# Kernel tuning notes

Measured on AMD Instinct MI355X. Metric: run time of the kernel, lower is better.

The kernel has to match this reference:

```python
import jax, jax.numpy as jnp
import numpy as np
from functools import partial

@jax.custom_vjp
def binarize(w):
    # BinaryConnectDeterministic forward: sign(w)
    return jnp.sign(w)

def _bin_fwd(w):
    return jnp.sign(w), w

def _bin_bwd(w, g):
    # straight-through estimator: pass grad where |w| <= 1
    return (g * (jnp.abs(w) <= 1.0).astype(g.dtype),)

binarize.defvjp(_bin_fwd, _bin_bwd)

STRIDE = (1, 1)
PADDING = ((1, 1), (1, 1))
DILATION = (1, 1)
GROUPS = 1

def setup_inputs() -> dict:
    key = jax.random.key(0)
    k1, k2, k3 = jax.random.split(key, 3)
    x = jax.random.normal(k1, (32, 256, 56, 56), dtype=jnp.float32)
    # uniform(-1, 1) init as in reset_parameters
    weight = jax.random.uniform(k2, (256, 256, 3, 3), dtype=jnp.float32, minval=-1.0, maxval=1.0)
    bias = jax.random.uniform(k3, (256,), dtype=jnp.float32, minval=-1.0, maxval=1.0)
    return {"x": x, "weight": weight, "bias": bias}

def reference(x, weight, bias):
    w_bin = binarize(weight)  # {-1, 0, +1} weights (sign)
    out = jax.lax.conv_general_dilated(
        x, w_bin,
        window_strides=STRIDE,
        padding=PADDING,
        rhs_dilation=DILATION,
        dimension_numbers=("NCHW", "OIHW", "NCHW"),
        feature_group_count=GROUPS,
    )
    return out + bias[None, :, None, None]
```

## Files before the change

kernel.cpp:

```cpp
#include <hip/hip_runtime.h>
#include <hip/hip_bf16.h>
#include <stdint.h>

#define N_IMG 32
#define C_IN  256
#define HW    56
#define PIX   3136
#define M_TOT 100352
#define C_OUT 256
#define K_TOT 2304
#define HP    58
#define WPAD  58
#define XPAD_ELEMS 27557888
#define OUT_IMG_STRIDE 802816

#define BM 224
#define BN 128
#define SLAB_PIX 348
#define SLAB_STRIDE 40

typedef __attribute__((ext_vector_type(8))) short bf16x8_t;
typedef __attribute__((ext_vector_type(4))) float f32x4_t;

__global__ void border_zero_kernel(__hip_bfloat16* __restrict__ xpad) {
    int t = blockIdx.x * 256 + threadIdx.x;
    if (t >= 32 * 228 * 32) return;
    int n = t / (228 * 32);
    int r = t - n * (228 * 32);
    int px = r >> 5, part = r & 31;
    int hp, wp;
    if (px < 58)       { hp = 0;  wp = px; }
    else if (px < 116) { hp = 57; wp = px - 116 + 58; }
    else { int k = px - 116; hp = 1 + (k >> 1); wp = (k & 1) ? 57 : 0; }
    long e = (((long)n * HP + hp) * WPAD + wp) * C_IN + part * 8;
    *(uint4*)(xpad + e) = make_uint4(0u, 0u, 0u, 0u);
}

__global__ void xform_kernel(const float* __restrict__ x, __hip_bfloat16* __restrict__ xpad) {
    __shared__ float tile[64][65];
    int b   = blockIdx.x;
    int n   = b / 196;
    int rem = b - n * 196;
    int ct  = rem / 49;
    int pt  = rem - ct * 49;
    int c0 = ct * 64, p0 = pt * 64;
    int t = threadIdx.x;

    const float* xs = x + (size_t)n * C_IN * PIX;
    int pc = t & 63, cr = t >> 6;
#pragma unroll
    for (int it = 0; it < 16; ++it) {
        int c = c0 + it * 4 + cr;
        tile[it * 4 + cr][pc] = xs[(size_t)c * PIX + p0 + pc];
    }
    __syncthreads();
    int cl = t & 63, pr = t >> 6;
#pragma unroll
    for (int it = 0; it < 16; ++it) {
        int p = p0 + it * 4 + pr;
        int h = p / HW, w = p - h * HW;
        float v = tile[cl][it * 4 + pr];
        xpad[(((size_t)n * HP + (h + 1)) * WPAD + (w + 1)) * C_IN + c0 + cl] = __float2bfloat16(v);
    }
}

__global__ void wxform_kernel(const float* __restrict__ w, __hip_bfloat16* __restrict__ wt) {
    int i = blockIdx.x * 256 + threadIdx.x;
    if (i >= C_OUT * K_TOT) return;
    int cout = i / K_TOT;
    int r    = i - cout * K_TOT;
    int tap  = r >> 8;
    int c    = r & 255;
    float v = w[cout * 2304 + c * 9 + tap];
    float s = (v > 0.f) ? 1.f : ((v < 0.f) ? -1.f : 0.f);
    wt[i] = __float2bfloat16(s);
}

__global__ void __launch_bounds__(256, 2)
gemm_kernel(const __hip_bfloat16* __restrict__ xpad,
            const __hip_bfloat16* __restrict__ wt,
            const float* __restrict__ bias,
            float* __restrict__ out) {
    __shared__ __hip_bfloat16 slab[SLAB_PIX * SLAB_STRIDE];

    int bx = blockIdx.x;
    int g = bx >> 4, xg = bx & 7, nt = (bx >> 3) & 1;
    int mt = g * 8 + xg;
    int nimg = mt / 14, ti = mt - nimg * 14;
    int r0 = ti * 4;
    int n0 = nt * BN;

    int tid = threadIdx.x, lane = tid & 63, wid = tid >> 6;
    int wm = wid >> 1, wn = wid & 1;
    int ar = lane & 15;
    int kq = lane >> 4;
    int kk = kq * 8;

    int ppb[7];
#pragma unroll
    for (int i = 0; i < 7; ++i) {
        int m = wm * 112 + i * 16 + ar;
        int dr = m / 56, wcol = m - dr * 56;
        ppb[i] = (dr * 58 + wcol) * (SLAB_STRIDE * 2) + kq * 16;
    }
    long wb[4];
#pragma unroll
    for (int j = 0; j < 4; ++j) {
        int n = n0 + wn * 64 + j * 16 + ar;
        wb[j] = (long)n * K_TOT + kk;
    }

    const __hip_bfloat16* srcBase = xpad + ((long)(nimg * HP + r0) * WPAD) * C_IN;

    f32x4_t acc[7][4] = {};

    for (int ch = 0; ch < 8; ++ch) {
        if (ch) __syncthreads();
#pragma unroll
        for (int it = 0; it < 6; ++it) {
            int s = it * 256 + tid;
            if (s < SLAB_PIX * 4) {
                int pp = s >> 2, part = s & 3;
                uint4 v = *(const uint4*)(srcBase + (long)pp * C_IN + ch * 32 + part * 8);
                *(uint4*)((char*)slab + pp * (SLAB_STRIDE * 2) + part * 16) = v;
            }
        }
        __syncthreads();

#pragma unroll
        for (int t = 0; t < 9; ++t) {
            const int kh = t / 3, kw = t - kh * 3;
            const int toff = (kh * 58 + kw) * (SLAB_STRIDE * 2);
            bf16x8_t b[4];
#pragma unroll
            for (int j = 0; j < 4; ++j)
                b[j] = *(const bf16x8_t*)&wt[wb[j] + t * 256 + ch * 32];
            bf16x8_t a[7];
#pragma unroll
            for (int i = 0; i < 7; ++i)
                a[i] = *(const bf16x8_t*)((const char*)slab + ppb[i] + toff);
#pragma unroll
            for (int i = 0; i < 7; ++i)
#pragma unroll
                for (int j = 0; j < 4; ++j)
                    acc[i][j] = __builtin_amdgcn_mfma_f32_16x16x32_bf16(a[i], b[j], acc[i][j], 0, 0, 0);
        }
    }

    int cn = lane & 15;
    int rq = (lane >> 4) * 4;
    long outb = (long)nimg * OUT_IMG_STRIDE + r0 * 56;
#pragma unroll
    for (int i = 0; i < 7; ++i) {
        int mb = wm * 112 + i * 16 + rq;
#pragma unroll
        for (int j = 0; j < 4; ++j) {
            int cout = n0 + wn * 64 + j * 16 + cn;
            float bv = bias[cout];
            f32x4_t v = acc[i][j];
            v[0] += bv; v[1] += bv; v[2] += bv; v[3] += bv;
            *(f32x4_t*)&out[outb + (long)cout * PIX + mb] = v;
        }
    }
}

extern "C" void kernel_launch(void* const* d_in, const int* in_sizes, int n_in,
                              void* d_out, int out_size, void* d_ws, size_t ws_size,
                              hipStream_t stream) {
    const float* x    = (const float*)d_in[0];
    const float* wgt  = (const float*)d_in[1];
    const float* bias = (const float*)d_in[2];
    float* out = (float*)d_out;

    __hip_bfloat16* xpad = (__hip_bfloat16*)d_ws;
    __hip_bfloat16* wt   = (__hip_bfloat16*)((char*)d_ws + 55115776);

    border_zero_kernel<<<dim3((32 * 228 * 32 + 255) / 256), dim3(256), 0, stream>>>(xpad);

    xform_kernel<<<dim3(N_IMG * 4 * 49), dim3(256), 0, stream>>>(x, xpad);

    wxform_kernel<<<dim3((C_OUT * K_TOT + 255) / 256), dim3(256), 0, stream>>>(wgt, wt);

    gemm_kernel<<<dim3((M_TOT / BM) * (C_OUT / BN)), dim3(256), 0, stream>>>(xpad, wt, bias, out);
}
```

Before: 348.8 us.

## Double-buffer input slab with register prefetch of next channel chunk

Makes the shared-memory input slab double-buffered. The next channel chunk is loaded from global into registers before the MFMA loop over the current chunk and written to the other buffer afterwards, so there is one barrier per chunk instead of two. The aim is to hide global-load latency behind the MFMA work. It costs 24 extra VGPRs for the prefetch and doubles LDS per block (about 55KB), which may reduce occupancy below the 2 blocks per CU set by the launch bounds.

```diff
diff --git a/kernel.cpp b/kernel.cpp
--- a/kernel.cpp
+++ b/kernel.cpp
@@ -18,6 +18,7 @@
 #define BN 128
 #define SLAB_PIX 348
 #define SLAB_STRIDE 40
+#define SLAB_ELEMS (SLAB_PIX * SLAB_STRIDE)
 
 typedef __attribute__((ext_vector_type(8))) short bf16x8_t;
 typedef __attribute__((ext_vector_type(4))) float f32x4_t;
@@ -81,7 +82,7 @@
             const __hip_bfloat16* __restrict__ wt,
             const float* __restrict__ bias,
             float* __restrict__ out) {
-    __shared__ __hip_bfloat16 slab[SLAB_PIX * SLAB_STRIDE];
+    __shared__ __hip_bfloat16 slab[2][SLAB_ELEMS];
 
     int bx = blockIdx.x;
     int g = bx >> 4, xg = bx & 7, nt = (bx >> 3) & 1;
@@ -114,19 +115,32 @@
 
     f32x4_t acc[7][4] = {};
 
+#pragma unroll
+    for (int it = 0; it < 6; ++it) {
+        int s = it * 256 + tid;
+        if (s < SLAB_PIX * 4) {
+            int pp = s >> 2, part = s & 3;
+            uint4 v = *(const uint4*)(srcBase + (long)pp * C_IN + part * 8);
+            *(uint4*)((char*)(&slab[0][0]) + pp * (SLAB_STRIDE * 2) + part * 16) = v;
+        }
+    }
+    __syncthreads();
+
+    int cur = 0;
     for (int ch = 0; ch < 8; ++ch) {
-        if (ch) __syncthreads();
-#pragma unroll
-        for (int it = 0; it < 6; ++it) {
-            int s = it * 256 + tid;
-            if (s < SLAB_PIX * 4) {
-                int pp = s >> 2, part = s & 3;
-                uint4 v = *(const uint4*)(srcBase + (long)pp * C_IN + ch * 32 + part * 8);
-                *(uint4*)((char*)slab + pp * (SLAB_STRIDE * 2) + part * 16) = v;
+        uint4 pref[6];
+        if (ch < 7) {
+#pragma unroll
+            for (int it = 0; it < 6; ++it) {
+                int s = it * 256 + tid;
+                if (s < SLAB_PIX * 4) {
+                    int pp = s >> 2, part = s & 3;
+                    pref[it] = *(const uint4*)(srcBase + (long)pp * C_IN + (ch + 1) * 32 + part * 8);
+                }
             }
         }
-        __syncthreads();
-
+
+        const char* sbase = (const char*)(&slab[cur][0]);
 #pragma unroll
         for (int t = 0; t < 9; ++t) {
             const int kh = t / 3, kw = t - kh * 3;
@@ -138,12 +152,25 @@
             bf16x8_t a[7];
 #pragma unroll
             for (int i = 0; i < 7; ++i)
-                a[i] = *(const bf16x8_t*)((const char*)slab + ppb[i] + toff);
+                a[i] = *(const bf16x8_t*)(sbase + ppb[i] + toff);
 #pragma unroll
             for (int i = 0; i < 7; ++i)
 #pragma unroll
                 for (int j = 0; j < 4; ++j)
                     acc[i][j] = __builtin_amdgcn_mfma_f32_16x16x32_bf16(a[i], b[j], acc[i][j], 0, 0, 0);
+        }
+
+        if (ch < 7) {
+#pragma unroll
+            for (int it = 0; it < 6; ++it) {
+                int s = it * 256 + tid;
+                if (s < SLAB_PIX * 4) {
+                    int pp = s >> 2, part = s & 3;
+                    *(uint4*)((char*)(&slab[cur ^ 1][0]) + pp * (SLAB_STRIDE * 2) + part * 16) = pref[it];
+                }
+            }
+            __syncthreads();
+            cur ^= 1;
         }
     }
 
```

Result: slower. 360.5 us (+3.4%).

## Double-buffer input slab with direct global-to-LDS loads and XOR swizzle

Applied to the files above, without the earlier changes.

Replaces the register-staged slab fill with a double-buffered LDS slab that is filled asynchronously through global_load_lds, prefetching the next channel chunk while MFMAs run on the current one. The padded-stride layout is replaced with an XOR swizzle to avoid bank conflicts. Weight fragments are software-prefetched one tap ahead, and instruction priority is raised around the MFMA block. The cost is extra per-tap barriers and hand-tuned vmcnt waits, which risk stalls or correctness problems if the counts are wrong.

```diff
diff --git a/kernel.cpp b/kernel.cpp
--- a/kernel.cpp
+++ b/kernel.cpp
@@ -11,13 +11,12 @@
 #define K_TOT 2304
 #define HP    58
 #define WPAD  58
-#define XPAD_ELEMS 27557888
 #define OUT_IMG_STRIDE 802816
 
 #define BM 224
 #define BN 128
 #define SLAB_PIX 348
-#define SLAB_STRIDE 40
+#define SLAB_SLOTS (SLAB_PIX * 4)
 
 typedef __attribute__((ext_vector_type(8))) short bf16x8_t;
 typedef __attribute__((ext_vector_type(4))) float f32x4_t;
@@ -81,7 +80,7 @@
             const __hip_bfloat16* __restrict__ wt,
             const float* __restrict__ bias,
             float* __restrict__ out) {
-    __shared__ __hip_bfloat16 slab[SLAB_PIX * SLAB_STRIDE];
+    __shared__ __hip_bfloat16 slab[2][SLAB_PIX * 32];
 
     int bx = blockIdx.x;
     int g = bx >> 4, xg = bx & 7, nt = (bx >> 3) & 1;
@@ -94,57 +93,104 @@
     int wm = wid >> 1, wn = wid & 1;
     int ar = lane & 15;
     int kq = lane >> 4;
-    int kk = kq * 8;
-
-    int ppb[7];
+
+    int p0[7];
 #pragma unroll
     for (int i = 0; i < 7; ++i) {
         int m = wm * 112 + i * 16 + ar;
         int dr = m / 56, wcol = m - dr * 56;
-        ppb[i] = (dr * 58 + wcol) * (SLAB_STRIDE * 2) + kq * 16;
+        p0[i] = dr * 58 + wcol;
     }
     long wb[4];
 #pragma unroll
     for (int j = 0; j < 4; ++j) {
         int n = n0 + wn * 64 + j * 16 + ar;
-        wb[j] = (long)n * K_TOT + kk;
+        wb[j] = (long)n * K_TOT + kq * 8;
     }
 
     const __hip_bfloat16* srcBase = xpad + ((long)(nimg * HP + r0) * WPAD) * C_IN;
 
     f32x4_t acc[7][4] = {};
 
+#pragma unroll
+    for (int it = 0; it < 6; ++it) {
+        int s = it * 256 + tid;
+        if (s < SLAB_SLOTS) {
+            int p = s >> 2, q = s & 3;
+            const __hip_bfloat16* gsrc = srcBase + (long)p * C_IN + ((q ^ ((p >> 1) & 3)) * 8);
+            __hip_bfloat16* ldst = &slab[0][(it * 256 + wid * 64) * 8];
+            __builtin_amdgcn_global_load_lds(
+                (const __attribute__((address_space(1))) void*)gsrc,
+                (__attribute__((address_space(3))) void*)ldst, 16, 0, 0);
+        }
+    }
+    bf16x8_t bcur[4];
+#pragma unroll
+    for (int j = 0; j < 4; ++j) bcur[j] = *(const bf16x8_t*)&wt[wb[j]];
+    __syncthreads();
+
+    int cur = 0;
     for (int ch = 0; ch < 8; ++ch) {
-        if (ch) __syncthreads();
-#pragma unroll
-        for (int it = 0; it < 6; ++it) {
-            int s = it * 256 + tid;
-            if (s < SLAB_PIX * 4) {
-                int pp = s >> 2, part = s & 3;
-                uint4 v = *(const uint4*)(srcBase + (long)pp * C_IN + ch * 32 + part * 8);
-                *(uint4*)((char*)slab + pp * (SLAB_STRIDE * 2) + part * 16) = v;
-            }
-        }
-        __syncthreads();
-
+        const __hip_bfloat16* sb = &slab[cur][0];
+        __hip_bfloat16* nb = &slab[cur ^ 1][0];
 #pragma unroll
         for (int t = 0; t < 9; ++t) {
             const int kh = t / 3, kw = t - kh * 3;
-            const int toff = (kh * 58 + kw) * (SLAB_STRIDE * 2);
-            bf16x8_t b[4];
-#pragma unroll
-            for (int j = 0; j < 4; ++j)
-                b[j] = *(const bf16x8_t*)&wt[wb[j] + t * 256 + ch * 32];
+            const int dpx = kh * 58 + kw;
+
             bf16x8_t a[7];
 #pragma unroll
+            for (int i = 0; i < 7; ++i) {
+                int p = p0[i] + dpx;
+                int off = (p << 5) + ((kq ^ ((p >> 1) & 3)) << 3);
+                a[i] = *(const bf16x8_t*)(sb + off);
+            }
+
+            if (ch < 7 && t < 6) {
+                int s = t * 256 + tid;
+                if (s < SLAB_SLOTS) {
+                    int p = s >> 2, q = s & 3;
+                    const __hip_bfloat16* gsrc =
+                        srcBase + (long)p * C_IN + (ch + 1) * 32 + ((q ^ ((p >> 1) & 3)) * 8);
+                    __hip_bfloat16* ldst = nb + (t * 256 + wid * 64) * 8;
+                    __builtin_amdgcn_global_load_lds(
+                        (const __attribute__((address_space(1))) void*)gsrc,
+                        (__attribute__((address_space(3))) void*)ldst, 16, 0, 0);
+                }
+            }
+
+            bf16x8_t bn[4];
+            const bool last = (ch == 7) && (t == 8);
+            if (!last) {
+                const int tn = (t < 8) ? t + 1 : 0;
+                const int cn = (t < 8) ? ch : ch + 1;
+#pragma unroll
+                for (int j = 0; j < 4; ++j)
+                    bn[j] = *(const bf16x8_t*)&wt[wb[j] + tn * 256 + cn * 32];
+            }
+
+            asm volatile("s_waitcnt vmcnt(5)");
+            __builtin_amdgcn_s_barrier();
+
+            __builtin_amdgcn_s_setprio(1);
+#pragma unroll
             for (int i = 0; i < 7; ++i)
-                a[i] = *(const bf16x8_t*)((const char*)slab + ppb[i] + toff);
-#pragma unroll
-            for (int i = 0; i < 7; ++i)
 #pragma unroll
                 for (int j = 0; j < 4; ++j)
-                    acc[i][j] = __builtin_amdgcn_mfma_f32_16x16x32_bf16(a[i], b[j], acc[i][j], 0, 0, 0);
+                    acc[i][j] = __builtin_amdgcn_mfma_f32_16x16x32_bf16(a[i], bcur[j], acc[i][j], 0, 0, 0);
+            __builtin_amdgcn_s_setprio(0);
+
+            if (t == 8) {
+                if (ch < 7) __syncthreads();
+            } else {
+                __builtin_amdgcn_s_barrier();
+            }
+            if (!last) {
+#pragma unroll
+                for (int j = 0; j < 4; ++j) bcur[j] = bn[j];
+            }
         }
+        cur ^= 1;
     }
 
     int cn = lane & 15;
```

After: 738.9 us. +111.8%, slower.
